# Performance work log

Measured on AMD Instinct MI355X. Metric: run time of the kernel, lower is better.

## Reference

```python
import jax, jax.numpy as jnp
import numpy as np

INPUT_SIZE = 1024
MODULE_SIZE = 256   # k
N_MODULES = 8       # g
HIDDEN = MODULE_SIZE * N_MODULES
T = 4096
PERIODS = jnp.array([2 ** i for i in range(N_MODULES)], dtype=jnp.int32)  # [1,2,...,128]


def setup_inputs() -> dict:
    key = jax.random.key(0)
    k1, k2, k3, k4, k5 = jax.random.split(key, 5)
    s = 1.0 / np.sqrt(HIDDEN)
    return {
        "x": jax.random.normal(k1, (T, INPUT_SIZE), dtype=jnp.float32),
        "W_ih": jax.random.normal(k2, (HIDDEN, INPUT_SIZE), dtype=jnp.float32) * s,
        "W_hh": jax.random.normal(k3, (HIDDEN, HIDDEN), dtype=jnp.float32) * s,
        "b_ih": jax.random.normal(k4, (HIDDEN,), dtype=jnp.float32) * s,
        "b_hh": jax.random.normal(k5, (HIDDEN,), dtype=jnp.float32) * s,
    }


def reference(x, W_ih, W_hh, b_ih, b_hh):
    # Clockwork RNN: at step t (1-indexed, curr_t starts at 1 for hx=None),
    # module j is active iff t % period_j == 0. Masking the weight columns
    # (rows of W^T) is equivalent to masking the pre-activation output, and
    # tanh(0)=0 so inactive modules keep their previous hidden value.
    ts = jnp.arange(1, x.shape[0] + 1, dtype=jnp.int32)

    def step(h, inp):
        xt, t = inp  # xt: (input_size,), t: scalar int
        mask = jnp.repeat((t % PERIODS) == 0, MODULE_SIZE).astype(h.dtype)  # (H,)
        pre = xt @ W_ih.T + b_ih + h @ W_hh.T + b_hh                        # (H,)
        h_new = h * (1.0 - mask) + jnp.tanh(pre * mask)
        return h_new, h_new

    h0 = jnp.zeros((HIDDEN,), dtype=x.dtype)
    _, outs = jax.lax.scan(step, h0, (x, ts))
    return outs  # (T, HIDDEN)
```

## Files before the change

### kernel.cpp

```cpp
#include <hip/hip_runtime.h>
#include <math.h>

#define T_STEPS 4096
#define HID     2048
#define MOD     256
#define INSZ    1024
#define NWAVE   256

static __device__ __forceinline__ unsigned long long agent_load_u64(
        const unsigned long long* p) {
    return __hip_atomic_load((unsigned long long*)p, __ATOMIC_RELAXED,
                             __HIP_MEMORY_SCOPE_AGENT);
}
static __device__ __forceinline__ void agent_store_u64(
        unsigned long long* p, unsigned long long v) {
    __hip_atomic_store(p, v, __ATOMIC_RELAXED, __HIP_MEMORY_SCOPE_AGENT);
}

#define BM 128
#define BN 128
#define BK 8

__global__ __launch_bounds__(256) void gemm_u(
    const float* __restrict__ x, const float* __restrict__ Wih,
    const float* __restrict__ bih, const float* __restrict__ bhh,
    float* __restrict__ out)
{
    __shared__ float As[BK][BM];
    __shared__ float Bs[BK][BN];

    const int tid = threadIdx.x;
    const int t0 = blockIdx.y * BM;
    const int i0 = blockIdx.x * BN;
    const int tx = tid & 15;
    const int ty = tid >> 4;
    const int arow = tid >> 1;
    const int acol = (tid & 1) * 4;

    float acc[8][8];
#pragma unroll
    for (int a = 0; a < 8; ++a)
#pragma unroll
        for (int b = 0; b < 8; ++b) acc[a][b] = 0.0f;

    for (int k0 = 0; k0 < INSZ; k0 += BK) {
        float4 av = *(const float4*)(x   + (size_t)(t0 + arow) * INSZ + k0 + acol);
        float4 bv = *(const float4*)(Wih + (size_t)(i0 + arow) * INSZ + k0 + acol);
        __syncthreads();
        As[acol + 0][arow] = av.x; As[acol + 1][arow] = av.y;
        As[acol + 2][arow] = av.z; As[acol + 3][arow] = av.w;
        Bs[acol + 0][arow] = bv.x; Bs[acol + 1][arow] = bv.y;
        Bs[acol + 2][arow] = bv.z; Bs[acol + 3][arow] = bv.w;
        __syncthreads();
#pragma unroll
        for (int kk = 0; kk < BK; ++kk) {
            float a[8], b[8];
            *(float4*)&a[0] = *(const float4*)&As[kk][ty * 8];
            *(float4*)&a[4] = *(const float4*)&As[kk][ty * 8 + 4];
            *(float4*)&b[0] = *(const float4*)&Bs[kk][tx * 8];
            *(float4*)&b[4] = *(const float4*)&Bs[kk][tx * 8 + 4];
#pragma unroll
            for (int ri = 0; ri < 8; ++ri)
#pragma unroll
                for (int ci = 0; ci < 8; ++ci)
                    acc[ri][ci] = fmaf(a[ri], b[ci], acc[ri][ci]);
        }
    }

    float bias[8];
#pragma unroll
    for (int ci = 0; ci < 8; ++ci) {
        int i = i0 + tx * 8 + ci;
        bias[ci] = bih[i] + bhh[i];
    }
#pragma unroll
    for (int ri = 0; ri < 8; ++ri) {
        int t = t0 + ty * 8 + ri;
#pragma unroll
        for (int ci = 0; ci < 8; ++ci) {
            int i = i0 + tx * 8 + ci;
            out[(size_t)t * HID + i] = acc[ri][ci] + bias[ci];
        }
    }
}

__global__ __launch_bounds__(64, 1) void cwrnn_rec(
    float* __restrict__ out, const float* __restrict__ Whh,
    unsigned long long* __restrict__ comm)
{
    const int lane = threadIdx.x;
    const int g    = blockIdx.x;

    float4 hreg[8];
#pragma unroll
    for (int j = 0; j < 8; ++j) hreg[j] = make_float4(0.f, 0.f, 0.f, 0.f);

    float4 w0[8];
    {
        const float4* wr = (const float4*)(Whh + (size_t)g * HID);
#pragma unroll
        for (int j = 0; j < 8; ++j) w0[j] = wr[lane + 64 * j];
    }

    for (int t = 1; t <= T_STEPS; ++t) {
        const int ctz = __builtin_ctz(t);
        const int A = (ctz + 1 > 8) ? 8 : (ctz + 1);
        float* orow = out + (size_t)(t - 1) * HID;

        float upf = (lane < A) ? orow[lane * MOD + g] : 0.0f;

        if (t > 1) {
            const int ctzp = __builtin_ctz(t - 1);
            const int Ap = (ctzp + 1 > 8) ? 8 : (ctzp + 1);
            const unsigned need = (unsigned)(t - 1);
            const unsigned long long* csrc =
                comm + (size_t)((t - 1) & 1) * HID + 4 * lane;
            unsigned long long pv[8][4];
            for (;;) {
#pragma unroll
                for (int j = 0; j < 8; ++j) {
                    if (j < Ap) {
                        pv[j][0] = agent_load_u64(csrc + j * MOD + 0);
                        pv[j][1] = agent_load_u64(csrc + j * MOD + 1);
                        pv[j][2] = agent_load_u64(csrc + j * MOD + 2);
                        pv[j][3] = agent_load_u64(csrc + j * MOD + 3);
                    }
                }
                bool ok = true;
#pragma unroll
                for (int j = 0; j < 8; ++j) {
                    if (j < Ap)
                        ok = ok && ((unsigned)(pv[j][0] >> 32) >= need)
                                && ((unsigned)(pv[j][1] >> 32) >= need)
                                && ((unsigned)(pv[j][2] >> 32) >= need)
                                && ((unsigned)(pv[j][3] >> 32) >= need);
                }
                if (ok) break;
            }
#pragma unroll
            for (int j = 0; j < 8; ++j) {
                if (j < Ap)
                    hreg[j] = make_float4(
                        __uint_as_float((unsigned)pv[j][0]),
                        __uint_as_float((unsigned)pv[j][1]),
                        __uint_as_float((unsigned)pv[j][2]),
                        __uint_as_float((unsigned)pv[j][3]));
            }
        }

        unsigned long long* cdst = comm + (size_t)(t & 1) * HID;
        const unsigned long long tagbits =
            ((unsigned long long)(unsigned)t) << 32;

        {
            float4 s = make_float4(0.f, 0.f, 0.f, 0.f);
#pragma unroll
            for (int j = 0; j < 8; ++j) {
                s.x = fmaf(w0[j].x, hreg[j].x, s.x);
                s.y = fmaf(w0[j].y, hreg[j].y, s.y);
                s.z = fmaf(w0[j].z, hreg[j].z, s.z);
                s.w = fmaf(w0[j].w, hreg[j].w, s.w);
            }
            float acc = (s.x + s.y) + (s.z + s.w);
#pragma unroll
            for (int off = 32; off; off >>= 1) acc += __shfl_xor(acc, off, 64);
            float u0 = __shfl(upf, 0, 64);
            if (lane == 0) {
                float hv = tanhf(u0 + acc);
                agent_store_u64(cdst + g,
                    tagbits | (unsigned long long)__float_as_uint(hv));
                orow[g] = hv;
            }
        }

        int m = 1;
        for (; m + 1 < A; m += 2) {
            const int ra = m * MOD + g;
            const int rb = ra + MOD;
            const float4* wa = (const float4*)(Whh + (size_t)ra * HID);
            const float4* wb = (const float4*)(Whh + (size_t)rb * HID);
            float4 sa = make_float4(0.f, 0.f, 0.f, 0.f);
            float4 sb = make_float4(0.f, 0.f, 0.f, 0.f);
#pragma unroll
            for (int j = 0; j < 8; ++j) {
                float4 a = wa[lane + 64 * j];
                float4 b = wb[lane + 64 * j];
                sa.x = fmaf(a.x, hreg[j].x, sa.x);
                sa.y = fmaf(a.y, hreg[j].y, sa.y);
                sa.z = fmaf(a.z, hreg[j].z, sa.z);
                sa.w = fmaf(a.w, hreg[j].w, sa.w);
                sb.x = fmaf(b.x, hreg[j].x, sb.x);
                sb.y = fmaf(b.y, hreg[j].y, sb.y);
                sb.z = fmaf(b.z, hreg[j].z, sb.z);
                sb.w = fmaf(b.w, hreg[j].w, sb.w);
            }
            float acca = (sa.x + sa.y) + (sa.z + sa.w);
            float accb = (sb.x + sb.y) + (sb.z + sb.w);
#pragma unroll
            for (int off = 32; off; off >>= 1) {
                acca += __shfl_xor(acca, off, 64);
                accb += __shfl_xor(accb, off, 64);
            }
            float ua = __shfl(upf, m, 64);
            float ub = __shfl(upf, m + 1, 64);
            if (lane == 0) {
                float hva = tanhf(ua + acca);
                float hvb = tanhf(ub + accb);
                agent_store_u64(cdst + ra,
                    tagbits | (unsigned long long)__float_as_uint(hva));
                agent_store_u64(cdst + rb,
                    tagbits | (unsigned long long)__float_as_uint(hvb));
                orow[ra] = hva;
                orow[rb] = hvb;
            }
        }
        if (m < A) {
            const int r = m * MOD + g;
            const float4* wr = (const float4*)(Whh + (size_t)r * HID);
            float4 s = make_float4(0.f, 0.f, 0.f, 0.f);
#pragma unroll
            for (int j = 0; j < 8; ++j) {
                float4 a = wr[lane + 64 * j];
                s.x = fmaf(a.x, hreg[j].x, s.x);
                s.y = fmaf(a.y, hreg[j].y, s.y);
                s.z = fmaf(a.z, hreg[j].z, s.z);
                s.w = fmaf(a.w, hreg[j].w, s.w);
            }
            float acc = (s.x + s.y) + (s.z + s.w);
#pragma unroll
            for (int off = 32; off; off >>= 1) acc += __shfl_xor(acc, off, 64);
            float um = __shfl(upf, m, 64);
            if (lane == 0) {
                float hv = tanhf(um + acc);
                agent_store_u64(cdst + r,
                    tagbits | (unsigned long long)__float_as_uint(hv));
                orow[r] = hv;
            }
        }

#pragma unroll
        for (int j = 0; j < 8; ++j) {
            if (j >= A && g == (j - A)) {
                *(float4*)(orow + j * MOD + 4 * lane) = hreg[j];
            }
        }
    }
}

extern "C" void kernel_launch(void* const* d_in, const int* in_sizes, int n_in,
                              void* d_out, int out_size, void* d_ws, size_t ws_size,
                              hipStream_t stream) {
    const float* x   = (const float*)d_in[0];
    const float* Wih = (const float*)d_in[1];
    const float* Whh = (const float*)d_in[2];
    const float* bih = (const float*)d_in[3];
    const float* bhh = (const float*)d_in[4];
    float* out = (float*)d_out;
    unsigned long long* comm = (unsigned long long*)d_ws;

    hipMemsetAsync(d_ws, 0, 2 * HID * sizeof(unsigned long long), stream);

    dim3 g1(HID / BN, T_STEPS / BM);
    gemm_u<<<g1, 256, 0, stream>>>(x, Wih, bih, bhh, out);
    cwrnn_rec<<<NWAVE, 64, 0, stream>>>(out, Whh, comm);
}
```

Measured before the change: 11.23 ms.

## Replicate module-0 recurrence per block and exchange slow-module deltas

Replaces the 256 single-wave blocks that synchronise every step through tagged global flags with 32 blocks of 1024 threads. Each block redundantly computes the period-1 module from register-resident weights and LDS state. The slower modules are split across blocks on even steps. Their contribution to module 0 is kept as a correction vector, updated incrementally from deltas and published once per two steps. The aim is to take the global spin-wait off odd steps and batch output writes through an LDS ring buffer, at the cost of duplicated work and much more complex synchronisation.

```diff
diff --git a/kernel.cpp b/kernel.cpp
--- a/kernel.cpp
+++ b/kernel.cpp
@@ -5,7 +5,11 @@
 #define HID     2048
 #define MOD     256
 #define INSZ    1024
-#define NWAVE   256
+
+#define NBLK 32
+#define NTHR 1024
+#define RPM  8
+#define NCE  8
 
 static __device__ __forceinline__ unsigned long long agent_load_u64(
         const unsigned long long* p) {
@@ -84,166 +88,230 @@
     }
 }
 
-__global__ __launch_bounds__(64, 1) void cwrnn_rec(
+__global__ __launch_bounds__(NTHR, 4) void cwrnn_rec(
     float* __restrict__ out, const float* __restrict__ Whh,
     unsigned long long* __restrict__ comm)
 {
-    const int lane = threadIdx.x;
-    const int g    = blockIdx.x;
-
-    float4 hreg[8];
-#pragma unroll
-    for (int j = 0; j < 8; ++j) hreg[j] = make_float4(0.f, 0.f, 0.f, 0.f);
-
-    float4 w0[8];
+    const int tid   = threadIdx.x;
+    const int b     = blockIdx.x;
+    const int lane  = tid & 63;
+    const int wave  = tid >> 6;
+    const int r4    = tid >> 4;
+    const int c16   = tid & 15;
+    const int rsel  = c16 & 3;
+    const int myrow = 4 * r4 + rsel;
+
+    unsigned long long* comm_h = comm;
+    unsigned long long* comm_c = comm + 7 * MOD;
+
+    __shared__ __align__(16) float lds_h[HID];
+    __shared__ __align__(16) float h0p[320];
+    __shared__ __align__(16) float lds_C[MOD];
+    __shared__ __align__(16) float lds_delta[7 * MOD];
+    __shared__ __align__(16) float lds_u0[MOD];
+    __shared__ __align__(16) float lds_ur[56];
+    __shared__ __align__(16) float lds_ring[3][64];
+    __shared__ float lds_red[NCE][2];
+
+    float4 w00[4][4];
+#pragma unroll
+    for (int rr = 0; rr < 4; ++rr) {
+        const float* wr = Whh + (size_t)(4 * r4 + rr) * HID + 16 * c16;
+#pragma unroll
+        for (int i = 0; i < 4; ++i) w00[rr][i] = *(const float4*)(wr + 4 * i);
+    }
+
+    for (int i = tid; i < HID; i += NTHR) lds_h[i] = 0.f;
+    if (tid < 320) h0p[tid] = 0.f;
+    if (tid < MOD) lds_C[tid] = 0.f;
+    if (tid < 56)  lds_ur[tid] = 0.f;
+    if (tid < 192) (&lds_ring[0][0])[tid] = 0.f;
+
     {
-        const float4* wr = (const float4*)(Whh + (size_t)g * HID);
-#pragma unroll
-        for (int j = 0; j < 8; ++j) w0[j] = wr[lane + 64 * j];
+        float4 u4 = make_float4(0.f, 0.f, 0.f, 0.f);
+        if (tid < 64) u4 = *(const float4*)(out + 4 * tid);
+        __syncthreads();
+        if (tid < 64) *(float4*)(lds_u0 + 4 * tid) = u4;
+        __syncthreads();
     }
 
     for (int t = 1; t <= T_STEPS; ++t) {
+        const bool ev = (t & 1) == 0;
         const int ctz = __builtin_ctz(t);
-        const int A = (ctz + 1 > 8) ? 8 : (ctz + 1);
-        float* orow = out + (size_t)(t - 1) * HID;
-
-        float upf = (lane < A) ? orow[lane * MOD + g] : 0.0f;
-
-        if (t > 1) {
-            const int ctzp = __builtin_ctz(t - 1);
-            const int Ap = (ctzp + 1 > 8) ? 8 : (ctzp + 1);
-            const unsigned need = (unsigned)(t - 1);
-            const unsigned long long* csrc =
-                comm + (size_t)((t - 1) & 1) * HID + 4 * lane;
-            unsigned long long pv[8][4];
-            for (;;) {
-#pragma unroll
-                for (int j = 0; j < 8; ++j) {
-                    if (j < Ap) {
-                        pv[j][0] = agent_load_u64(csrc + j * MOD + 0);
-                        pv[j][1] = agent_load_u64(csrc + j * MOD + 1);
-                        pv[j][2] = agent_load_u64(csrc + j * MOD + 2);
-                        pv[j][3] = agent_load_u64(csrc + j * MOD + 3);
-                    }
-                }
-                bool ok = true;
-#pragma unroll
-                for (int j = 0; j < 8; ++j) {
-                    if (j < Ap)
-                        ok = ok && ((unsigned)(pv[j][0] >> 32) >= need)
-                                && ((unsigned)(pv[j][1] >> 32) >= need)
-                                && ((unsigned)(pv[j][2] >> 32) >= need)
-                                && ((unsigned)(pv[j][3] >> 32) >= need);
-                }
-                if (ok) break;
-            }
-#pragma unroll
-            for (int j = 0; j < 8; ++j) {
-                if (j < Ap)
-                    hreg[j] = make_float4(
-                        __uint_as_float((unsigned)pv[j][0]),
-                        __uint_as_float((unsigned)pv[j][1]),
-                        __uint_as_float((unsigned)pv[j][2]),
-                        __uint_as_float((unsigned)pv[j][3]));
-            }
-        }
-
-        unsigned long long* cdst = comm + (size_t)(t & 1) * HID;
+        const int j   = ev ? (ctz < 7 ? ctz : 7) : 0;
         const unsigned long long tagbits =
             ((unsigned long long)(unsigned)t) << 32;
 
-        {
-            float4 s = make_float4(0.f, 0.f, 0.f, 0.f);
-#pragma unroll
-            for (int j = 0; j < 8; ++j) {
-                s.x = fmaf(w0[j].x, hreg[j].x, s.x);
-                s.y = fmaf(w0[j].y, hreg[j].y, s.y);
-                s.z = fmaf(w0[j].z, hreg[j].z, s.z);
-                s.w = fmaf(w0[j].w, hreg[j].w, s.w);
-            }
-            float acc = (s.x + s.y) + (s.z + s.w);
-#pragma unroll
-            for (int off = 32; off; off >>= 1) acc += __shfl_xor(acc, off, 64);
-            float u0 = __shfl(upf, 0, 64);
-            if (lane == 0) {
-                float hv = tanhf(u0 + acc);
-                agent_store_u64(cdst + g,
-                    tagbits | (unsigned long long)__float_as_uint(hv));
-                orow[g] = hv;
-            }
-        }
-
-        int m = 1;
-        for (; m + 1 < A; m += 2) {
-            const int ra = m * MOD + g;
-            const int rb = ra + MOD;
-            const float4* wa = (const float4*)(Whh + (size_t)ra * HID);
-            const float4* wb = (const float4*)(Whh + (size_t)rb * HID);
-            float4 sa = make_float4(0.f, 0.f, 0.f, 0.f);
-            float4 sb = make_float4(0.f, 0.f, 0.f, 0.f);
-#pragma unroll
-            for (int j = 0; j < 8; ++j) {
-                float4 a = wa[lane + 64 * j];
-                float4 b = wb[lane + 64 * j];
-                sa.x = fmaf(a.x, hreg[j].x, sa.x);
-                sa.y = fmaf(a.y, hreg[j].y, sa.y);
-                sa.z = fmaf(a.z, hreg[j].z, sa.z);
-                sa.w = fmaf(a.w, hreg[j].w, sa.w);
-                sb.x = fmaf(b.x, hreg[j].x, sb.x);
-                sb.y = fmaf(b.y, hreg[j].y, sb.y);
-                sb.z = fmaf(b.z, hreg[j].z, sb.z);
-                sb.w = fmaf(b.w, hreg[j].w, sb.w);
-            }
-            float acca = (sa.x + sa.y) + (sa.z + sa.w);
-            float accb = (sb.x + sb.y) + (sb.z + sb.w);
-#pragma unroll
-            for (int off = 32; off; off >>= 1) {
-                acca += __shfl_xor(acca, off, 64);
-                accb += __shfl_xor(accb, off, 64);
-            }
-            float ua = __shfl(upf, m, 64);
-            float ub = __shfl(upf, m + 1, 64);
-            if (lane == 0) {
-                float hva = tanhf(ua + acca);
-                float hvb = tanhf(ub + accb);
-                agent_store_u64(cdst + ra,
-                    tagbits | (unsigned long long)__float_as_uint(hva));
-                agent_store_u64(cdst + rb,
-                    tagbits | (unsigned long long)__float_as_uint(hvb));
-                orow[ra] = hva;
-                orow[rb] = hvb;
-            }
-        }
-        if (m < A) {
-            const int r = m * MOD + g;
-            const float4* wr = (const float4*)(Whh + (size_t)r * HID);
-            float4 s = make_float4(0.f, 0.f, 0.f, 0.f);
-#pragma unroll
-            for (int j = 0; j < 8; ++j) {
-                float4 a = wr[lane + 64 * j];
-                s.x = fmaf(a.x, hreg[j].x, s.x);
-                s.y = fmaf(a.y, hreg[j].y, s.y);
-                s.z = fmaf(a.z, hreg[j].z, s.z);
-                s.w = fmaf(a.w, hreg[j].w, s.w);
-            }
-            float acc = (s.x + s.y) + (s.z + s.w);
-#pragma unroll
-            for (int off = 32; off; off >>= 1) acc += __shfl_xor(acc, off, 64);
-            float um = __shfl(upf, m, 64);
-            if (lane == 0) {
-                float hv = tanhf(um + acc);
-                agent_store_u64(cdst + r,
-                    tagbits | (unsigned long long)__float_as_uint(hv));
-                orow[r] = hv;
-            }
-        }
-
-#pragma unroll
-        for (int j = 0; j < 8; ++j) {
-            if (j >= A && g == (j - A)) {
-                *(float4*)(orow + j * MOD + 4 * lane) = hreg[j];
-            }
-        }
+        const float uval = lds_u0[myrow];
+        if (t >= 3 && tid < 16) {
+            float4 e4 = *(const float4*)(&lds_ring[(t + 1) % 3][4 * tid]);
+            *(float4*)(out + (size_t)(t - 3) * HID + 64 * b + 4 * tid) = e4;
+        }
+        float4 pf0 = make_float4(0.f, 0.f, 0.f, 0.f);
+        float4 pfr = make_float4(0.f, 0.f, 0.f, 0.f);
+        if (t < T_STEPS) {
+            if (tid < 64)
+                pf0 = *(const float4*)(out + (size_t)t * HID + 4 * tid);
+            if (!ev && tid >= 64 && tid < 78) {
+                const int idx = tid - 64, mm = idx >> 1, dd = idx & 1;
+                pfr = *(const float4*)(out + (size_t)t * HID
+                                       + (mm + 1) * MOD + RPM * b + 4 * dd);
+            }
+        }
+
+        if (ev) {
+            for (int ridx = wave; ridx < RPM * j; ridx += 16) {
+                const int m = 1 + (ridx >> 3);
+                const int e = ridx & 7;
+                const float* wrow = Whh + (size_t)(m * MOD + RPM * b + e) * HID;
+                float4 wv[8];
+#pragma unroll
+                for (int k = 0; k < 8; ++k)
+                    wv[k] = *(const float4*)(wrow + 4 * lane + 256 * k);
+                float sx = 0.f, sy = 0.f, sz = 0.f, sw = 0.f;
+#pragma unroll
+                for (int k = 0; k < 8; ++k) {
+                    const float4 hv = *(const float4*)(lds_h + 4 * lane + 256 * k);
+                    sx = fmaf(wv[k].x, hv.x, sx);
+                    sy = fmaf(wv[k].y, hv.y, sy);
+                    sz = fmaf(wv[k].z, hv.z, sz);
+                    sw = fmaf(wv[k].w, hv.w, sw);
+                }
+                float acc = (sx + sy) + (sz + sw);
+#pragma unroll
+                for (int off = 32; off; off >>= 1)
+                    acc += __shfl_xor(acc, off, 64);
+                if (lane == 0) {
+                    const float hv = tanhf(lds_ur[(m - 1) * 8 + e] + acc);
+                    agent_store_u64(comm_h + (m - 1) * MOD + RPM * b + e,
+                        tagbits | (unsigned long long)__float_as_uint(hv));
+                }
+            }
+        }
+
+        float a0 = 0.f, a1 = 0.f, a2 = 0.f, a3 = 0.f;
+#pragma unroll
+        for (int i = 0; i < 4; ++i) {
+            const float4 hv = *(const float4*)(h0p + 20 * c16 + 4 * i);
+            a0 = fmaf(w00[0][i].x, hv.x, a0); a0 = fmaf(w00[0][i].y, hv.y, a0);
+            a0 = fmaf(w00[0][i].z, hv.z, a0); a0 = fmaf(w00[0][i].w, hv.w, a0);
+            a1 = fmaf(w00[1][i].x, hv.x, a1); a1 = fmaf(w00[1][i].y, hv.y, a1);
+            a1 = fmaf(w00[1][i].z, hv.z, a1); a1 = fmaf(w00[1][i].w, hv.w, a1);
+            a2 = fmaf(w00[2][i].x, hv.x, a2); a2 = fmaf(w00[2][i].y, hv.y, a2);
+            a2 = fmaf(w00[2][i].z, hv.z, a2); a2 = fmaf(w00[2][i].w, hv.w, a2);
+            a3 = fmaf(w00[3][i].x, hv.x, a3); a3 = fmaf(w00[3][i].y, hv.y, a3);
+            a3 = fmaf(w00[3][i].z, hv.z, a3); a3 = fmaf(w00[3][i].w, hv.w, a3);
+        }
+#pragma unroll
+        for (int off = 1; off <= 8; off <<= 1) {
+            a0 += __shfl_xor(a0, off, 64);
+            a1 += __shfl_xor(a1, off, 64);
+            a2 += __shfl_xor(a2, off, 64);
+            a3 += __shfl_xor(a3, off, 64);
+        }
+        const float pre = (rsel == 0) ? a0 : (rsel == 1) ? a1
+                        : (rsel == 2) ? a2 : a3;
+
+        if (!ev) {
+            if (tid < MOD) {
+                const unsigned need = (unsigned)(t - 1);
+                unsigned long long pv;
+                do { pv = agent_load_u64(comm_c + tid); }
+                while ((unsigned)(pv >> 32) < need);
+                lds_C[tid] = __uint_as_float((unsigned)pv);
+            }
+            __syncthreads();
+            const float hv_new = tanhf(uval + lds_C[myrow] + pre);
+            if (c16 < 4) {
+                lds_h[myrow] = hv_new;
+                h0p[myrow + (myrow >> 4) * 4] = hv_new;
+                if (b < 4 && (myrow >> 6) == b)
+                    lds_ring[t % 3][myrow & 63] = hv_new;
+            }
+            if (b >= 4 && tid < 16)
+                *(float4*)(&lds_ring[t % 3][4 * tid]) =
+                    *(const float4*)(&lds_ring[(t + 2) % 3][4 * tid]);
+            if (t < T_STEPS) {
+                if (tid < 64) *(float4*)(lds_u0 + 4 * tid) = pf0;
+                if (tid >= 64 && tid < 78) {
+                    const int idx = tid - 64;
+                    *(float4*)(lds_ur + (idx >> 1) * 8 + 4 * (idx & 1)) = pfr;
+                }
+            }
+            __syncthreads();
+        } else {
+            const float hv_new = tanhf(uval + lds_C[myrow] + pre);
+            __syncthreads();
+            if (c16 < 4) {
+                lds_h[myrow] = hv_new;
+                h0p[myrow + (myrow >> 4) * 4] = hv_new;
+                if (b < 4 && (myrow >> 6) == b)
+                    lds_ring[t % 3][myrow & 63] = hv_new;
+            }
+            const int nslot = j * MOD;
+            {
+                const unsigned need = (unsigned)t;
+                const int s0 = tid, s1 = tid + NTHR;
+                const bool w0 = s0 < nslot, w1 = s1 < nslot;
+                unsigned long long p0 = 0, p1 = 0;
+                if (w0 | w1) {
+                    for (;;) {
+                        if (w0) p0 = agent_load_u64(comm_h + s0);
+                        if (w1) p1 = agent_load_u64(comm_h + s1);
+                        if ((!w0 || (unsigned)(p0 >> 32) >= need) &&
+                            (!w1 || (unsigned)(p1 >> 32) >= need)) break;
+                    }
+                }
+                const int base = 64 * b - MOD;
+                if (w0) {
+                    const float v = __uint_as_float((unsigned)p0);
+                    lds_delta[s0] = v - lds_h[MOD + s0];
+                    lds_h[MOD + s0] = v;
+                    if (b >= 4 && s0 >= base && s0 < base + 64)
+                        lds_ring[t % 3][s0 - base] = v;
+                }
+                if (w1) {
+                    const float v = __uint_as_float((unsigned)p1);
+                    lds_delta[s1] = v - lds_h[MOD + s1];
+                    lds_h[MOD + s1] = v;
+                    if (b >= 4 && s1 >= base && s1 < base + 64)
+                        lds_ring[t % 3][s1 - base] = v;
+                }
+            }
+            if (b >= 4 && (b >> 2) > j && tid < 16)
+                *(float4*)(&lds_ring[t % 3][4 * tid]) =
+                    *(const float4*)(&lds_ring[(t + 2) % 3][4 * tid]);
+            if (t < T_STEPS && tid < 64)
+                *(float4*)(lds_u0 + 4 * tid) = pf0;
+            __syncthreads();
+            {
+                const int e   = tid >> 7;
+                const int sub = tid & 127;
+                const float* wc = Whh + (size_t)(NCE * b + e) * HID + MOD;
+                float acc = 0.f;
+                for (int kk = sub; kk < nslot; kk += 128)
+                    acc = fmaf(wc[kk], lds_delta[kk], acc);
+#pragma unroll
+                for (int off = 32; off; off >>= 1)
+                    acc += __shfl_xor(acc, off, 64);
+                if (lane == 0) lds_red[e][(tid >> 6) & 1] = acc;
+            }
+            __syncthreads();
+            if (tid < NCE) {
+                const int gi = NCE * b + tid;
+                const float cn = lds_C[gi] + lds_red[tid][0] + lds_red[tid][1];
+                agent_store_u64(comm_c + gi,
+                    tagbits | (unsigned long long)__float_as_uint(cn));
+            }
+        }
+    }
+
+    __syncthreads();
+    if (tid < 16) {
+        *(float4*)(out + (size_t)(T_STEPS - 2) * HID + 64 * b + 4 * tid) =
+            *(const float4*)(&lds_ring[(T_STEPS - 1) % 3][4 * tid]);
+        *(float4*)(out + (size_t)(T_STEPS - 1) * HID + 64 * b + 4 * tid) =
+            *(const float4*)(&lds_ring[T_STEPS % 3][4 * tid]);
     }
 }
 
@@ -258,9 +326,9 @@
     float* out = (float*)d_out;
     unsigned long long* comm = (unsigned long long*)d_ws;
 
-    hipMemsetAsync(d_ws, 0, 2 * HID * sizeof(unsigned long long), stream);
+    hipMemsetAsync(d_ws, 0, (7 * MOD + MOD) * sizeof(unsigned long long), stream);
 
     dim3 g1(HID / BN, T_STEPS / BM);
     gemm_u<<<g1, 256, 0, stream>>>(x, Wih, bih, bhh, out);
-    cwrnn_rec<<<NWAVE, 64, 0, stream>>>(out, Whh, comm);
-}
+    cwrnn_rec<<<NBLK, NTHR, 0, stream>>>(out, Whh, comm);
+}
```

Measured after the change: 22.81 ms. 2.03x slower.
